# Performance work log

Measured on AMD Instinct MI355X. Metric: run time of the kernel, lower is better.

Reference implementation:

```python
import jax, jax.numpy as jnp
import numpy as np

EPS = 1e-6
NEG_SLOPE = 0.2


def setup_inputs() -> dict:
    key = jax.random.key(0)
    k1, k2 = jax.random.split(key)
    B, D, T = 4, 512, 2048
    H, Dh = 8, 512 // 8
    x = jax.random.normal(k1, (B, D, T), dtype=jnp.float32)
    qkv = jax.random.normal(k2, (3, H, D, Dh), dtype=jnp.float32) * 0.02
    norm_w = jnp.ones((1,), dtype=jnp.float32)
    return {"x": x, "qkv": qkv, "norm_w": norm_w}


def reference(x, qkv, norm_w):
    B, D, T = x.shape
    H = qkv.shape[1]
    # leaky relu on channels-first input
    x = jnp.where(x >= 0, x, NEG_SLOPE * x)
    # fused QKV projection: (B,D,T),(3,H,D,Dh) -> (3,B,H,T,Dh)
    h = jnp.einsum('bdt,nhdD->nbhtD', x, qkv)
    # RMSNorm over the sequence axis (dim=-2), scalar learned weight
    denom = jnp.mean(h * h, axis=-2, keepdims=True)
    h = norm_w * (h / jnp.sqrt(denom + EPS))
    q, k, v = h[0], h[1], h[2]
    scale = jnp.sqrt(jnp.asarray(D // H, dtype=x.dtype))
    # manual attention: (B,H,T,T) score matrix
    attn = jax.nn.softmax(jnp.einsum('bhtD,bhTD->bhtT', q, k) / scale, axis=-1)
    # weighted values, output laid out (B,H,Dh,T) then merged to (B,D,T)
    out = jnp.einsum('bhtT,bhTD->bhDt', attn, v)
    return out.reshape(B, D, T)
```

## Files before the change

kernel.cpp:

```cpp
#include <hip/hip_runtime.h>
#include <cstddef>

#define B   4
#define D   512
#define T   2048
#define H   8
#define DH  64
#define NEG_SLOPE 0.2f
#define EPS 1e-6f
#define LOG2E 1.44269504088896340736f

typedef __attribute__((ext_vector_type(8))) short short8;
typedef __attribute__((ext_vector_type(4))) float float4v;

__device__ __forceinline__ float bf2f(ushort u) {
    unsigned int x = ((unsigned int)u) << 16;
    return __builtin_bit_cast(float, x);
}
__device__ __forceinline__ ushort f2bf(float f) {
    unsigned int x = __builtin_bit_cast(unsigned int, f);
    x = x + 0x7fffu + ((x >> 16) & 1u);
    return (ushort)(x >> 16);
}

__global__ __launch_bounds__(256) void transpose_lrelu(const float* __restrict__ src,
                                                       ushort* __restrict__ dst,
                                                       int src_ld, int dst_ld,
                                                       size_t src_mstride, size_t dst_mstride,
                                                       int do_lrelu,
                                                       float* __restrict__ zbuf, int zcount) {
    const int tid = threadIdx.x;
    if (zbuf != nullptr && blockIdx.x == 0 && blockIdx.y == 0 && blockIdx.z == 0) {
        for (int i = tid; i < zcount; i += 256) zbuf[i] = 0.f;
    }

    const int c0 = blockIdx.x * 64, r0 = blockIdx.y * 64;
    const float* s = src + blockIdx.z * src_mstride + (size_t)r0 * src_ld + c0;
    ushort*      d = dst + blockIdx.z * dst_mstride + (size_t)c0 * dst_ld + r0;

    __shared__ float Ls[64][68];

    const int rl = tid >> 4, c4 = (tid & 15) * 4;
    #pragma unroll
    for (int p = 0; p < 4; ++p) {
        float4 v = *(const float4*)(s + (size_t)(rl + p * 16) * src_ld + c4);
        if (do_lrelu) {
            v.x = fmaxf(v.x, NEG_SLOPE * v.x);
            v.y = fmaxf(v.y, NEG_SLOPE * v.y);
            v.z = fmaxf(v.z, NEG_SLOPE * v.z);
            v.w = fmaxf(v.w, NEG_SLOPE * v.w);
        }
        *(float4*)&Ls[rl + p * 16][c4] = v;
    }
    __syncthreads();

    const int tl = tid >> 2;
    #pragma unroll
    for (int it = 0; it < 2; ++it) {
        int ch = (tid & 3) + it * 4;
        ushort o[8];
        #pragma unroll
        for (int j = 0; j < 8; ++j) o[j] = f2bf(Ls[ch * 8 + j][tl]);
        *(uint4*)(d + (size_t)tl * dst_ld + ch * 8) = *(uint4*)o;
    }
}

__global__ __launch_bounds__(256) void qkv_mm(const ushort* __restrict__ xT,
                                              const ushort* __restrict__ WT,
                                              ushort* __restrict__ hb,
                                              ushort* __restrict__ vT,
                                              float* __restrict__ ssq) {
    const int tid = threadIdx.x, wave = tid >> 6, lane = tid & 63;
    const int quad = lane >> 4, l16 = lane & 15;
    const int wr = wave >> 1, wc = wave & 1;
    const int t0  = blockIdx.x * 128;
    const int gd0 = blockIdx.y * 128;
    const int b   = blockIdx.z;

    __shared__ ushort SMEM[2 * 128 * 64];
    ushort* At = SMEM;
    ushort* Bt = SMEM + 128 * 64;

    const ushort* xb = xT + (size_t)b * T * D + (size_t)t0 * D;
    const ushort* wb = WT + (size_t)gd0 * D;

    const int srow = lane >> 3;
    const int csrc = (lane & 7) ^ srow;

    const bool is_v = (blockIdx.y >= 8);
    const ushort* Asrc = is_v ? At : Bt;
    const ushort* Bsrc = is_v ? Bt : At;
    const int arow0 = is_v ? wr * 64 : wc * 64;
    const int brow0 = is_v ? wc * 64 : wr * 64;

    float4v acc[4][4];
    #pragma unroll
    for (int i = 0; i < 4; ++i)
        #pragma unroll
        for (int j = 0; j < 4; ++j) acc[i][j] = (float4v){0.f, 0.f, 0.f, 0.f};

    for (int k0 = 0; k0 < D; k0 += 64) {
        #pragma unroll
        for (int i = 0; i < 4; ++i) {
            int rbase = wave * 32 + i * 8;
            int row = rbase + srow;
            const ushort* ga = xb + (size_t)row * D + k0 + csrc * 8;
            const ushort* gb = wb + (size_t)row * D + k0 + csrc * 8;
            __builtin_amdgcn_global_load_lds(
                (const __attribute__((address_space(1))) unsigned int*)ga,
                (__attribute__((address_space(3))) unsigned int*)&At[rbase * 64], 16, 0, 0);
            __builtin_amdgcn_global_load_lds(
                (const __attribute__((address_space(1))) unsigned int*)gb,
                (__attribute__((address_space(3))) unsigned int*)&Bt[rbase * 64], 16, 0, 0);
        }
        __syncthreads();

        #pragma unroll
        for (int kh = 0; kh < 2; ++kh) {
            short8 aF[4], bF[4];
            #pragma unroll
            for (int mt = 0; mt < 4; ++mt) {
                int row = arow0 + mt * 16 + l16;
                aF[mt] = *(const short8*)&Asrc[row * 64 + (((kh * 4 + quad) ^ (l16 & 7)) * 8)];
            }
            #pragma unroll
            for (int nt = 0; nt < 4; ++nt) {
                int row = brow0 + nt * 16 + l16;
                bF[nt] = *(const short8*)&Bsrc[row * 64 + (((kh * 4 + quad) ^ (l16 & 7)) * 8)];
            }
            #pragma unroll
            for (int mt = 0; mt < 4; ++mt)
                #pragma unroll
                for (int nt = 0; nt < 4; ++nt)
                    acc[mt][nt] = __builtin_amdgcn_mfma_f32_16x16x32_bf16(
                        aF[mt], bF[nt], acc[mt][nt], 0, 0, 0);
        }
        __syncthreads();
    }

    const int g  = blockIdx.y * 2 + wc;
    const int n  = g >> 3, hh = g & 7;
    const int ch = ((n * B + b) * H + hh) * 64;

    ushort* E = SMEM + wave * 4096;

    #pragma unroll
    for (int mt = 0; mt < 4; ++mt) {
        #pragma unroll
        for (int nt = 0; nt < 4; ++nt) {
            float4v c = acc[mt][nt];
            ushort4 pk;
            pk.x = f2bf(c[0]); pk.y = f2bf(c[1]);
            pk.z = f2bf(c[2]); pk.w = f2bf(c[3]);
            int row   = nt * 16 + l16;
            int chunk = mt * 2 + (quad >> 1);
            int pos   = chunk ^ (l16 & 7);
            *(ushort4*)&E[row * 64 + pos * 8 + (quad & 1) * 4] = pk;
        }
    }

    const int rsub = lane >> 3;
    const int csub = lane & 7;
    const int posr = csub ^ rsub;

    if (!is_v) {
        ushort* hbase = hb + (((size_t)n * B + b) * H + hh) * (size_t)T * DH
                        + (size_t)(t0 + wr * 64) * DH;
        float sq8[8] = {0.f, 0.f, 0.f, 0.f, 0.f, 0.f, 0.f, 0.f};
        #pragma unroll
        for (int i = 0; i < 8; ++i) {
            uint4 v = *(const uint4*)&E[(i * 8 + rsub) * 64 + posr * 8];
            const ushort* u = (const ushort*)&v;
            #pragma unroll
            for (int j = 0; j < 8; ++j) { float f = bf2f(u[j]); sq8[j] += f * f; }
            *(uint4*)(hbase + (size_t)(i * 8 + rsub) * DH + csub * 8) = v;
        }
        #pragma unroll
        for (int j = 0; j < 8; ++j) {
            float s = sq8[j];
            s += __shfl_xor(s, 8); s += __shfl_xor(s, 16); s += __shfl_xor(s, 32);
            if (lane < 8) atomicAdd(&ssq[ch + lane * 8 + j], s);
        }
    } else {
        ushort* vbase = vT + ((size_t)b * H + hh) * (size_t)DH * T + (t0 + wr * 64);
        #pragma unroll
        for (int i = 0; i < 8; ++i) {
            uint4 v = *(const uint4*)&E[(i * 8 + rsub) * 64 + posr * 8];
            const ushort* u = (const ushort*)&v;
            float s = 0.f;
            #pragma unroll
            for (int j = 0; j < 8; ++j) { float f = bf2f(u[j]); s += f * f; }
            *(uint4*)(vbase + (size_t)(i * 8 + rsub) * T + csub * 8) = v;
            s += __shfl_xor(s, 1); s += __shfl_xor(s, 2); s += __shfl_xor(s, 4);
            if ((lane & 7) == 0) atomicAdd(&ssq[ch + i * 8 + rsub], s);
        }
    }
}

__global__ __launch_bounds__(256, 4) void flash_attn(const ushort* __restrict__ hb,
                                                     const ushort* __restrict__ vT,
                                                     const float* __restrict__ ssq,
                                                     const float* __restrict__ norm_w,
                                                     float* __restrict__ out) {
    const int tid  = threadIdx.x;
    const int wave = tid >> 6;
    const int lane = tid & 63;
    const int quad = lane >> 4;
    const int l16  = lane & 15;

    const int lin  = blockIdx.x;
    const int head = ((lin & 7) << 2) | ((lin >> 3) & 3);
    const int t0   = (lin >> 5) * 64;
    const int b    = head >> 3, hh = head & 7;

    const size_t slab = (size_t)B * H * T * DH;
    const ushort* qp = hb + (size_t)head * T * DH;
    const ushort* kp = hb + slab + (size_t)head * T * DH;
    const ushort* vp = vT + (size_t)head * DH * T;

    __shared__ ushort Kt[64 * 64];
    __shared__ ushort Vt[64 * 64];
    __shared__ ushort Pb[4][16 * 64];
    __shared__ float fqk[64], sv[64];

    if (tid < 64) {
        float nw = norm_w[0];
        float mq = ssq[(0 * B * H + head) * 64 + tid] * (1.0f / T) + EPS;
        float mk = ssq[(1 * B * H + head) * 64 + tid] * (1.0f / T) + EPS;
        float mv = ssq[(2 * B * H + head) * 64 + tid] * (1.0f / T) + EPS;
        fqk[tid] = nw * nw * rsqrtf(mq) * rsqrtf(mk) * 0.125f * LOG2E;
        sv[tid]  = nw * rsqrtf(mv);
    }
    __syncthreads();

    short8 bQ[2];
    {
        const ushort* qr = qp + (size_t)(t0 + wave * 16 + l16) * DH;
        #pragma unroll
        for (int kh = 0; kh < 2; ++kh) {
            short8 raw = *(const short8*)(qr + kh * 32 + quad * 8);
            #pragma unroll
            for (int j = 0; j < 8; ++j) {
                float f = bf2f((ushort)raw[j]) * fqk[kh * 32 + quad * 8 + j];
                bQ[kh][j] = (short)f2bf(f);
            }
        }
    }

    const int srow = lane >> 3;
    const int csrc = (lane & 7) ^ srow;
    const ushort* kA = kp + (size_t)(wave * 16 + srow) * DH + csrc * 8;
    const ushort* kB = kp + (size_t)(wave * 16 + 8 + srow) * DH + csrc * 8;
    const ushort* vA = vp + (size_t)(wave * 16 + srow) * T + csrc * 8;
    const ushort* vB = vp + (size_t)(wave * 16 + 8 + srow) * T + csrc * 8;

    float l_run = 0.f;
    float4v O[4];
    #pragma unroll
    for (int dt = 0; dt < 4; ++dt) O[dt] = (float4v){0.f, 0.f, 0.f, 0.f};

    for (int j0 = 0; j0 < T; j0 += 64) {
        __builtin_amdgcn_global_load_lds(
            (const __attribute__((address_space(1))) unsigned int*)(kA + (size_t)j0 * DH),
            (__attribute__((address_space(3))) unsigned int*)&Kt[(wave * 16) * 64], 16, 0, 0);
        __builtin_amdgcn_global_load_lds(
            (const __attribute__((address_space(1))) unsigned int*)(kB + (size_t)j0 * DH),
            (__attribute__((address_space(3))) unsigned int*)&Kt[(wave * 16 + 8) * 64], 16, 0, 0);
        __builtin_amdgcn_global_load_lds(
            (const __attribute__((address_space(1))) unsigned int*)(vA + j0),
            (__attribute__((address_space(3))) unsigned int*)&Vt[(wave * 16) * 64], 16, 0, 0);
        __builtin_amdgcn_global_load_lds(
            (const __attribute__((address_space(1))) unsigned int*)(vB + j0),
            (__attribute__((address_space(3))) unsigned int*)&Vt[(wave * 16 + 8) * 64], 16, 0, 0);
        __syncthreads();

        float4v S[4];
        #pragma unroll
        for (int mt = 0; mt < 4; ++mt) S[mt] = (float4v){0.f, 0.f, 0.f, 0.f};
        #pragma unroll
        for (int kh = 0; kh < 2; ++kh) {
            #pragma unroll
            for (int mt = 0; mt < 4; ++mt) {
                int row = mt * 16 + l16;
                short8 aK = *(const short8*)&Kt[row * 64 + (((kh * 4 + quad) ^ (row & 7)) * 8)];
                S[mt] = __builtin_amdgcn_mfma_f32_16x16x32_bf16(aK, bQ[kh], S[mt], 0, 0, 0);
            }
        }

        #pragma unroll
        for (int mt = 0; mt < 4; ++mt) {
            float p0 = __builtin_amdgcn_exp2f(S[mt][0]);
            float p1 = __builtin_amdgcn_exp2f(S[mt][1]);
            float p2 = __builtin_amdgcn_exp2f(S[mt][2]);
            float p3 = __builtin_amdgcn_exp2f(S[mt][3]);
            l_run += (p0 + p1) + (p2 + p3);
            unsigned int a0 = __builtin_bit_cast(unsigned int, p0) + 0x8000u;
            unsigned int a1 = __builtin_bit_cast(unsigned int, p1) + 0x8000u;
            unsigned int a2 = __builtin_bit_cast(unsigned int, p2) + 0x8000u;
            unsigned int a3 = __builtin_bit_cast(unsigned int, p3) + 0x8000u;
            uint2 pk;
            pk.x = __builtin_amdgcn_perm(a1, a0, 0x07060302u);
            pk.y = __builtin_amdgcn_perm(a3, a2, 0x07060302u);
            *(uint2*)&Pb[wave][l16 * 64 + (((mt * 2 + (quad >> 1)) ^ (l16 & 7)) * 8)
                               + (quad & 1) * 4] = pk;
        }

        #pragma unroll
        for (int kh = 0; kh < 2; ++kh) {
            short8 bP = *(const short8*)&Pb[wave][l16 * 64 + (((kh * 4 + quad) ^ (l16 & 7)) * 8)];
            #pragma unroll
            for (int dt = 0; dt < 4; ++dt) {
                int row = dt * 16 + l16;
                short8 aV = *(const short8*)&Vt[row * 64 + (((kh * 4 + quad) ^ (row & 7)) * 8)];
                O[dt] = __builtin_amdgcn_mfma_f32_16x16x32_bf16(aV, bP, O[dt], 0, 0, 0);
            }
        }
        __syncthreads();
    }

    float rs = l_run;
    rs += __shfl_xor(rs, 16);
    rs += __shfl_xor(rs, 32);
    float inv = 1.f / rs;
    const int t = t0 + wave * 16 + l16;
    #pragma unroll
    for (int dt = 0; dt < 4; ++dt) {
        #pragma unroll
        for (int r = 0; r < 4; ++r) {
            int dd = dt * 16 + quad * 4 + r;
            out[((size_t)b * D + hh * DH + dd) * T + t] = O[dt][r] * inv * sv[dd];
        }
    }
}

extern "C" void kernel_launch(void* const* d_in, const int* in_sizes, int n_in,
                              void* d_out, int out_size, void* d_ws, size_t ws_size,
                              hipStream_t stream) {
    const float* x      = (const float*)d_in[0];
    const float* qkv    = (const float*)d_in[1];
    const float* norm_w = (const float*)d_in[2];
    float* out = (float*)d_out;

    const size_t HB_BYTES = (size_t)2 * B * H * T * DH * 2;
    const size_t VT_BYTES = (size_t)B * H * DH * T * 2;
    const size_t XT_BYTES = (size_t)B * T * D * 2;
    const size_t WT_BYTES = (size_t)3 * H * DH * D * 2;
    ushort* hb  = (ushort*)d_ws;
    ushort* vT  = (ushort*)((char*)d_ws + HB_BYTES);
    ushort* xT  = (ushort*)((char*)d_ws + HB_BYTES + VT_BYTES);
    ushort* WT  = (ushort*)((char*)d_ws + HB_BYTES + VT_BYTES + XT_BYTES);
    float*  ssq = (float*)((char*)d_ws + HB_BYTES + VT_BYTES + XT_BYTES + WT_BYTES);
    const int SSQ_N = 3 * B * H * DH;

    transpose_lrelu<<<dim3(T / 64, D / 64, B), 256, 0, stream>>>(
        x, xT, T, D, (size_t)D * T, (size_t)T * D, 1, ssq, SSQ_N);
    transpose_lrelu<<<dim3(DH / 64, D / 64, 3 * H), 256, 0, stream>>>(
        qkv, WT, DH, D, (size_t)D * DH, (size_t)DH * D, 0, nullptr, 0);

    qkv_mm<<<dim3(T / 128, (3 * H * DH) / 128, B), 256, 0, stream>>>(xT, WT, hb, vT, ssq);
    flash_attn<<<dim3((T / 64) * B * H), 256, 0, stream>>>(hb, vT, ssq, norm_w, out);
}
```

Baseline: 156.3 us.

## Double-buffer GEMM and attention tiles, widen attention query tile, fuse transposes

Merges the two transpose launches into one kernel that indexes by blockIdx.z, so weight blocks with blockIdx.x != 0 exit early. Double-buffers the K-loop LDS tiles in the QKV GEMM and the K/V tiles in flash attention, issuing the next tile's loads before computing on the current one. Flash attention now handles 128 queries per block (32 per wave), so each K/V tile is reused across two query groups and the grid halves. The cost is more LDS and more registers per block, and the launch bound drops its occupancy hint of 4, which may reduce occupancy.

```diff
diff --git a/kernel.cpp b/kernel.cpp
--- a/kernel.cpp
+++ b/kernel.cpp
@@ -23,23 +23,35 @@
     return (ushort)(x >> 16);
 }
 
-__global__ __launch_bounds__(256) void transpose_lrelu(const float* __restrict__ src,
-                                                       ushort* __restrict__ dst,
-                                                       int src_ld, int dst_ld,
-                                                       size_t src_mstride, size_t dst_mstride,
-                                                       int do_lrelu,
-                                                       float* __restrict__ zbuf, int zcount) {
+__global__ __launch_bounds__(256) void transpose_fused(const float* __restrict__ x,
+                                                       const float* __restrict__ qkv,
+                                                       ushort* __restrict__ xT,
+                                                       ushort* __restrict__ WT,
+                                                       float* __restrict__ ssq, int zcount) {
     const int tid = threadIdx.x;
-    if (zbuf != nullptr && blockIdx.x == 0 && blockIdx.y == 0 && blockIdx.z == 0) {
-        for (int i = tid; i < zcount; i += 256) zbuf[i] = 0.f;
-    }
-
-    const int c0 = blockIdx.x * 64, r0 = blockIdx.y * 64;
-    const float* s = src + blockIdx.z * src_mstride + (size_t)r0 * src_ld + c0;
-    ushort*      d = dst + blockIdx.z * dst_mstride + (size_t)c0 * dst_ld + r0;
+    const int z = blockIdx.z;
+    if (z == 0 && blockIdx.x == 0 && blockIdx.y == 0) {
+        for (int i = tid; i < zcount; i += 256) ssq[i] = 0.f;
+    }
+
+    const float* s;
+    ushort* d;
+    int src_ld, dst_ld, do_lrelu;
+    if (z < B) {
+        const int c0 = blockIdx.x * 64, r0 = blockIdx.y * 64;
+        s = x + (size_t)z * D * T + (size_t)r0 * T + c0;
+        d = xT + (size_t)z * T * D + (size_t)c0 * D + r0;
+        src_ld = T; dst_ld = D; do_lrelu = 1;
+    } else {
+        if (blockIdx.x != 0) return;
+        const int g = z - B;
+        const int r0 = blockIdx.y * 64;
+        s = qkv + (size_t)g * D * DH + (size_t)r0 * DH;
+        d = WT + (size_t)g * DH * D + r0;
+        src_ld = DH; dst_ld = D; do_lrelu = 0;
+    }
 
     __shared__ float Ls[64][68];
-
     const int rl = tid >> 4, c4 = (tid & 15) * 4;
     #pragma unroll
     for (int p = 0; p < 4; ++p) {
@@ -77,21 +89,14 @@
     const int gd0 = blockIdx.y * 128;
     const int b   = blockIdx.z;
 
-    __shared__ ushort SMEM[2 * 128 * 64];
-    ushort* At = SMEM;
-    ushort* Bt = SMEM + 128 * 64;
+    __shared__ ushort SMEM[4 * 8192];
 
     const ushort* xb = xT + (size_t)b * T * D + (size_t)t0 * D;
     const ushort* wb = WT + (size_t)gd0 * D;
 
     const int srow = lane >> 3;
     const int csrc = (lane & 7) ^ srow;
-
     const bool is_v = (blockIdx.y >= 8);
-    const ushort* Asrc = is_v ? At : Bt;
-    const ushort* Bsrc = is_v ? Bt : At;
-    const int arow0 = is_v ? wr * 64 : wc * 64;
-    const int brow0 = is_v ? wc * 64 : wr * 64;
 
     float4v acc[4][4];
     #pragma unroll
@@ -99,21 +104,46 @@
         #pragma unroll
         for (int j = 0; j < 4; ++j) acc[i][j] = (float4v){0.f, 0.f, 0.f, 0.f};
 
-    for (int k0 = 0; k0 < D; k0 += 64) {
+    {
+        ushort* At = SMEM;
+        ushort* Bt = SMEM + 8192;
         #pragma unroll
         for (int i = 0; i < 4; ++i) {
             int rbase = wave * 32 + i * 8;
             int row = rbase + srow;
-            const ushort* ga = xb + (size_t)row * D + k0 + csrc * 8;
-            const ushort* gb = wb + (size_t)row * D + k0 + csrc * 8;
-            __builtin_amdgcn_global_load_lds(
-                (const __attribute__((address_space(1))) unsigned int*)ga,
+            __builtin_amdgcn_global_load_lds(
+                (const __attribute__((address_space(1))) unsigned int*)(xb + (size_t)row * D + csrc * 8),
                 (__attribute__((address_space(3))) unsigned int*)&At[rbase * 64], 16, 0, 0);
             __builtin_amdgcn_global_load_lds(
-                (const __attribute__((address_space(1))) unsigned int*)gb,
+                (const __attribute__((address_space(1))) unsigned int*)(wb + (size_t)row * D + csrc * 8),
                 (__attribute__((address_space(3))) unsigned int*)&Bt[rbase * 64], 16, 0, 0);
         }
+    }
+
+    for (int ks = 0; ks < 8; ++ks) {
         __syncthreads();
+        if (ks < 7) {
+            int k0 = (ks + 1) * 64;
+            ushort* At = SMEM + ((ks + 1) & 1) * 16384;
+            ushort* Bt = At + 8192;
+            #pragma unroll
+            for (int i = 0; i < 4; ++i) {
+                int rbase = wave * 32 + i * 8;
+                int row = rbase + srow;
+                __builtin_amdgcn_global_load_lds(
+                    (const __attribute__((address_space(1))) unsigned int*)(xb + (size_t)row * D + k0 + csrc * 8),
+                    (__attribute__((address_space(3))) unsigned int*)&At[rbase * 64], 16, 0, 0);
+                __builtin_amdgcn_global_load_lds(
+                    (const __attribute__((address_space(1))) unsigned int*)(wb + (size_t)row * D + k0 + csrc * 8),
+                    (__attribute__((address_space(3))) unsigned int*)&Bt[rbase * 64], 16, 0, 0);
+            }
+        }
+        const ushort* At = SMEM + (ks & 1) * 16384;
+        const ushort* Bt = At + 8192;
+        const ushort* Asrc = is_v ? At : Bt;
+        const ushort* Bsrc = is_v ? Bt : At;
+        const int arow0 = is_v ? wr * 64 : wc * 64;
+        const int brow0 = is_v ? wc * 64 : wr * 64;
 
         #pragma unroll
         for (int kh = 0; kh < 2; ++kh) {
@@ -135,13 +165,11 @@
                     acc[mt][nt] = __builtin_amdgcn_mfma_f32_16x16x32_bf16(
                         aF[mt], bF[nt], acc[mt][nt], 0, 0, 0);
         }
-        __syncthreads();
     }
 
     const int g  = blockIdx.y * 2 + wc;
     const int n  = g >> 3, hh = g & 7;
     const int ch = ((n * B + b) * H + hh) * 64;
-
     ushort* E = SMEM + wave * 4096;
 
     #pragma unroll
@@ -197,11 +225,11 @@
     }
 }
 
-__global__ __launch_bounds__(256, 4) void flash_attn(const ushort* __restrict__ hb,
-                                                     const ushort* __restrict__ vT,
-                                                     const float* __restrict__ ssq,
-                                                     const float* __restrict__ norm_w,
-                                                     float* __restrict__ out) {
+__global__ __launch_bounds__(256) void flash_attn(const ushort* __restrict__ hb,
+                                                  const ushort* __restrict__ vT,
+                                                  const float* __restrict__ ssq,
+                                                  const float* __restrict__ norm_w,
+                                                  float* __restrict__ out) {
     const int tid  = threadIdx.x;
     const int wave = tid >> 6;
     const int lane = tid & 63;
@@ -210,7 +238,7 @@
 
     const int lin  = blockIdx.x;
     const int head = ((lin & 7) << 2) | ((lin >> 3) & 3);
-    const int t0   = (lin >> 5) * 64;
+    const int t0   = (lin >> 5) * 128;
     const int b    = head >> 3, hh = head & 7;
 
     const size_t slab = (size_t)B * H * T * DH;
@@ -218,9 +246,9 @@
     const ushort* kp = hb + slab + (size_t)head * T * DH;
     const ushort* vp = vT + (size_t)head * DH * T;
 
-    __shared__ ushort Kt[64 * 64];
-    __shared__ ushort Vt[64 * 64];
-    __shared__ ushort Pb[4][16 * 64];
+    __shared__ ushort Kt[2][64 * 64];
+    __shared__ ushort Vt[2][64 * 64];
+    __shared__ ushort Pb[4][32 * 64];
     __shared__ float fqk[64], sv[64];
 
     if (tid < 64) {
@@ -233,16 +261,17 @@
     }
     __syncthreads();
 
-    short8 bQ[2];
-    {
-        const ushort* qr = qp + (size_t)(t0 + wave * 16 + l16) * DH;
+    short8 bQ[2][2];
+    #pragma unroll
+    for (int qg = 0; qg < 2; ++qg) {
+        const ushort* qr = qp + (size_t)(t0 + wave * 32 + qg * 16 + l16) * DH;
         #pragma unroll
         for (int kh = 0; kh < 2; ++kh) {
             short8 raw = *(const short8*)(qr + kh * 32 + quad * 8);
             #pragma unroll
             for (int j = 0; j < 8; ++j) {
                 float f = bf2f((ushort)raw[j]) * fqk[kh * 32 + quad * 8 + j];
-                bQ[kh][j] = (short)f2bf(f);
+                bQ[qg][kh][j] = (short)f2bf(f);
             }
         }
     }
@@ -254,81 +283,119 @@
     const ushort* vA = vp + (size_t)(wave * 16 + srow) * T + csrc * 8;
     const ushort* vB = vp + (size_t)(wave * 16 + 8 + srow) * T + csrc * 8;
 
-    float l_run = 0.f;
-    float4v O[4];
-    #pragma unroll
-    for (int dt = 0; dt < 4; ++dt) O[dt] = (float4v){0.f, 0.f, 0.f, 0.f};
-
-    for (int j0 = 0; j0 < T; j0 += 64) {
+    float l_run[2] = {0.f, 0.f};
+    float4v O[2][4];
+    #pragma unroll
+    for (int qg = 0; qg < 2; ++qg)
+        #pragma unroll
+        for (int dt = 0; dt < 4; ++dt) O[qg][dt] = (float4v){0.f, 0.f, 0.f, 0.f};
+
+    {
         __builtin_amdgcn_global_load_lds(
-            (const __attribute__((address_space(1))) unsigned int*)(kA + (size_t)j0 * DH),
-            (__attribute__((address_space(3))) unsigned int*)&Kt[(wave * 16) * 64], 16, 0, 0);
+            (const __attribute__((address_space(1))) unsigned int*)kA,
+            (__attribute__((address_space(3))) unsigned int*)&Kt[0][(wave * 16) * 64], 16, 0, 0);
         __builtin_amdgcn_global_load_lds(
-            (const __attribute__((address_space(1))) unsigned int*)(kB + (size_t)j0 * DH),
-            (__attribute__((address_space(3))) unsigned int*)&Kt[(wave * 16 + 8) * 64], 16, 0, 0);
+            (const __attribute__((address_space(1))) unsigned int*)kB,
+            (__attribute__((address_space(3))) unsigned int*)&Kt[0][(wave * 16 + 8) * 64], 16, 0, 0);
         __builtin_amdgcn_global_load_lds(
-            (const __attribute__((address_space(1))) unsigned int*)(vA + j0),
-            (__attribute__((address_space(3))) unsigned int*)&Vt[(wave * 16) * 64], 16, 0, 0);
+            (const __attribute__((address_space(1))) unsigned int*)vA,
+            (__attribute__((address_space(3))) unsigned int*)&Vt[0][(wave * 16) * 64], 16, 0, 0);
         __builtin_amdgcn_global_load_lds(
-            (const __attribute__((address_space(1))) unsigned int*)(vB + j0),
-            (__attribute__((address_space(3))) unsigned int*)&Vt[(wave * 16 + 8) * 64], 16, 0, 0);
+            (const __attribute__((address_space(1))) unsigned int*)vB,
+            (__attribute__((address_space(3))) unsigned int*)&Vt[0][(wave * 16 + 8) * 64], 16, 0, 0);
+    }
+
+    for (int jt = 0; jt < 32; ++jt) {
         __syncthreads();
-
-        float4v S[4];
-        #pragma unroll
-        for (int mt = 0; mt < 4; ++mt) S[mt] = (float4v){0.f, 0.f, 0.f, 0.f};
+        if (jt < 31) {
+            const int p = (jt + 1) & 1;
+            const size_t jk = (size_t)(jt + 1) * 64;
+            __builtin_amdgcn_global_load_lds(
+                (const __attribute__((address_space(1))) unsigned int*)(kA + jk * DH),
+                (__attribute__((address_space(3))) unsigned int*)&Kt[p][(wave * 16) * 64], 16, 0, 0);
+            __builtin_amdgcn_global_load_lds(
+                (const __attribute__((address_space(1))) unsigned int*)(kB + jk * DH),
+                (__attribute__((address_space(3))) unsigned int*)&Kt[p][(wave * 16 + 8) * 64], 16, 0, 0);
+            __builtin_amdgcn_global_load_lds(
+                (const __attribute__((address_space(1))) unsigned int*)(vA + jk),
+                (__attribute__((address_space(3))) unsigned int*)&Vt[p][(wave * 16) * 64], 16, 0, 0);
+            __builtin_amdgcn_global_load_lds(
+                (const __attribute__((address_space(1))) unsigned int*)(vB + jk),
+                (__attribute__((address_space(3))) unsigned int*)&Vt[p][(wave * 16 + 8) * 64], 16, 0, 0);
+        }
+        const int p = jt & 1;
+
+        float4v S[2][4];
+        #pragma unroll
+        for (int qg = 0; qg < 2; ++qg)
+            #pragma unroll
+            for (int mt = 0; mt < 4; ++mt) S[qg][mt] = (float4v){0.f, 0.f, 0.f, 0.f};
         #pragma unroll
         for (int kh = 0; kh < 2; ++kh) {
             #pragma unroll
             for (int mt = 0; mt < 4; ++mt) {
                 int row = mt * 16 + l16;
-                short8 aK = *(const short8*)&Kt[row * 64 + (((kh * 4 + quad) ^ (row & 7)) * 8)];
-                S[mt] = __builtin_amdgcn_mfma_f32_16x16x32_bf16(aK, bQ[kh], S[mt], 0, 0, 0);
-            }
-        }
-
-        #pragma unroll
-        for (int mt = 0; mt < 4; ++mt) {
-            float p0 = __builtin_amdgcn_exp2f(S[mt][0]);
-            float p1 = __builtin_amdgcn_exp2f(S[mt][1]);
-            float p2 = __builtin_amdgcn_exp2f(S[mt][2]);
-            float p3 = __builtin_amdgcn_exp2f(S[mt][3]);
-            l_run += (p0 + p1) + (p2 + p3);
-            unsigned int a0 = __builtin_bit_cast(unsigned int, p0) + 0x8000u;
-            unsigned int a1 = __builtin_bit_cast(unsigned int, p1) + 0x8000u;
-            unsigned int a2 = __builtin_bit_cast(unsigned int, p2) + 0x8000u;
-            unsigned int a3 = __builtin_bit_cast(unsigned int, p3) + 0x8000u;
-            uint2 pk;
-            pk.x = __builtin_amdgcn_perm(a1, a0, 0x07060302u);
-            pk.y = __builtin_amdgcn_perm(a3, a2, 0x07060302u);
-            *(uint2*)&Pb[wave][l16 * 64 + (((mt * 2 + (quad >> 1)) ^ (l16 & 7)) * 8)
-                               + (quad & 1) * 4] = pk;
+                short8 aK = *(const short8*)&Kt[p][row * 64 + (((kh * 4 + quad) ^ (row & 7)) * 8)];
+                #pragma unroll
+                for (int qg = 0; qg < 2; ++qg)
+                    S[qg][mt] = __builtin_amdgcn_mfma_f32_16x16x32_bf16(aK, bQ[qg][kh], S[qg][mt], 0, 0, 0);
+            }
+        }
+
+        #pragma unroll
+        for (int qg = 0; qg < 2; ++qg) {
+            #pragma unroll
+            for (int mt = 0; mt < 4; ++mt) {
+                float p0 = __builtin_amdgcn_exp2f(S[qg][mt][0]);
+                float p1 = __builtin_amdgcn_exp2f(S[qg][mt][1]);
+                float p2 = __builtin_amdgcn_exp2f(S[qg][mt][2]);
+                float p3 = __builtin_amdgcn_exp2f(S[qg][mt][3]);
+                l_run[qg] += (p0 + p1) + (p2 + p3);
+                unsigned int a0 = __builtin_bit_cast(unsigned int, p0) + 0x8000u;
+                unsigned int a1 = __builtin_bit_cast(unsigned int, p1) + 0x8000u;
+                unsigned int a2 = __builtin_bit_cast(unsigned int, p2) + 0x8000u;
+                unsigned int a3 = __builtin_bit_cast(unsigned int, p3) + 0x8000u;
+                uint2 pk;
+                pk.x = __builtin_amdgcn_perm(a1, a0, 0x07060302u);
+                pk.y = __builtin_amdgcn_perm(a3, a2, 0x07060302u);
+                *(uint2*)&Pb[wave][(qg * 16 + l16) * 64
+                                   + (((mt * 2 + (quad >> 1)) ^ (l16 & 7)) * 8)
+                                   + (quad & 1) * 4] = pk;
+            }
         }
 
         #pragma unroll
         for (int kh = 0; kh < 2; ++kh) {
-            short8 bP = *(const short8*)&Pb[wave][l16 * 64 + (((kh * 4 + quad) ^ (l16 & 7)) * 8)];
+            short8 bP[2];
+            #pragma unroll
+            for (int qg = 0; qg < 2; ++qg)
+                bP[qg] = *(const short8*)&Pb[wave][(qg * 16 + l16) * 64
+                                                   + (((kh * 4 + quad) ^ (l16 & 7)) * 8)];
             #pragma unroll
             for (int dt = 0; dt < 4; ++dt) {
                 int row = dt * 16 + l16;
-                short8 aV = *(const short8*)&Vt[row * 64 + (((kh * 4 + quad) ^ (row & 7)) * 8)];
-                O[dt] = __builtin_amdgcn_mfma_f32_16x16x32_bf16(aV, bP, O[dt], 0, 0, 0);
-            }
-        }
-        __syncthreads();
-    }
-
-    float rs = l_run;
-    rs += __shfl_xor(rs, 16);
-    rs += __shfl_xor(rs, 32);
-    float inv = 1.f / rs;
-    const int t = t0 + wave * 16 + l16;
-    #pragma unroll
-    for (int dt = 0; dt < 4; ++dt) {
-        #pragma unroll
-        for (int r = 0; r < 4; ++r) {
-            int dd = dt * 16 + quad * 4 + r;
-            out[((size_t)b * D + hh * DH + dd) * T + t] = O[dt][r] * inv * sv[dd];
+                short8 aV = *(const short8*)&Vt[p][row * 64 + (((kh * 4 + quad) ^ (row & 7)) * 8)];
+                #pragma unroll
+                for (int qg = 0; qg < 2; ++qg)
+                    O[qg][dt] = __builtin_amdgcn_mfma_f32_16x16x32_bf16(aV, bP[qg], O[qg][dt], 0, 0, 0);
+            }
+        }
+    }
+
+    #pragma unroll
+    for (int qg = 0; qg < 2; ++qg) {
+        float rs = l_run[qg];
+        rs += __shfl_xor(rs, 16);
+        rs += __shfl_xor(rs, 32);
+        float inv = 1.f / rs;
+        const int t = t0 + wave * 32 + qg * 16 + l16;
+        #pragma unroll
+        for (int dt = 0; dt < 4; ++dt) {
+            #pragma unroll
+            for (int r = 0; r < 4; ++r) {
+                int dd = dt * 16 + quad * 4 + r;
+                out[((size_t)b * D + hh * DH + dd) * T + t] = O[qg][dt][r] * inv * sv[dd];
+            }
         }
     }
 }
@@ -352,11 +419,8 @@
     float*  ssq = (float*)((char*)d_ws + HB_BYTES + VT_BYTES + XT_BYTES + WT_BYTES);
     const int SSQ_N = 3 * B * H * DH;
 
-    transpose_lrelu<<<dim3(T / 64, D / 64, B), 256, 0, stream>>>(
-        x, xT, T, D, (size_t)D * T, (size_t)T * D, 1, ssq, SSQ_N);
-    transpose_lrelu<<<dim3(DH / 64, D / 64, 3 * H), 256, 0, stream>>>(
-        qkv, WT, DH, D, (size_t)D * DH, (size_t)DH * D, 0, nullptr, 0);
-
+    transpose_fused<<<dim3(T / 64, D / 64, B + 3 * H), 256, 0, stream>>>(
+        x, qkv, xT, WT, ssq, SSQ_N);
     qkv_mm<<<dim3(T / 128, (3 * H * DH) / 128, B), 256, 0, stream>>>(xT, WT, hb, vT, ssq);
-    flash_attn<<<dim3((T / 64) * B * H), 256, 0, stream>>>(hb, vT, ssq, norm_w, out);
-}
+    flash_attn<<<dim3((T / 128) * B * H), 256, 0, stream>>>(hb, vT, ssq, norm_w, out);
+}
```

Result: slower. 171.0 us (+9.4%).
